# Optimization experiments

Hardware: AMD Instinct MI355X
Metric: run time of the kernel (lower is better)

The kernel has to match this reference:

```python
import jax, jax.numpy as jnp
import numpy as np

P = 16          # patch size (patch_height == patch_width)
DIM = 768       # feature dim
K = 9           # number of anchor boxes (arange(0, 9) in source)
# anchor_boxes = [(h_ratio, w_ratio) for h in (2,4,8) for w in (2,4,8)]
BOX_H = jnp.array([2., 2., 2., 4., 4., 4., 8., 8., 8.], dtype=jnp.float32)
BOX_W = jnp.array([2., 4., 8., 2., 4., 8., 2., 4., 8.], dtype=jnp.float32)


def setup_inputs() -> dict:
    key = jax.random.key(0)
    k0, k1, k2, k3 = jax.random.split(key, 4)
    b, c, h, w = 32, 3, 512, 512
    img = jax.random.normal(k0, (b, c, h, w), dtype=jnp.float32)
    # patch-embed stand-in for feature_extraction_ViT: (c*P*P) -> DIM
    w_patch = jax.random.normal(k1, (c * P * P, DIM), dtype=jnp.float32) * 0.02
    w_reg = jax.random.normal(k2, (DIM, 4 * K), dtype=jnp.float32) * 0.02
    b_reg = jnp.zeros((4 * K,), dtype=jnp.float32)
    w_obj = jax.random.normal(k3, (DIM, K), dtype=jnp.float32) * 0.02
    b_obj = jnp.zeros((K,), dtype=jnp.float32)
    return {"img": img, "w_patch": w_patch, "w_reg": w_reg, "b_reg": b_reg,
            "w_obj": w_obj, "b_obj": b_obj}


def reference(img, w_patch, w_reg, b_reg, w_obj, b_obj):
    b, c, h, w = img.shape
    fh, fw = h // P, w // P
    # --- feature_extraction_ViT (patch embedding) -> feature map [b, fh, fw, DIM]
    patches = img.reshape(b, c, fh, P, fw, P).transpose(0, 2, 4, 1, 3, 5)
    patches = patches.reshape(b, fh, fw, c * P * P)
    feat = patches @ w_patch                                  # [b, fh, fw, DIM]
    # --- RPN: regs [b, fh, fw, K, 4], objectness [b, fh, fw, K, 1]
    regs = (feat @ w_reg + b_reg).reshape(b, fh, fw, K, 4)    # separate_anchor_boxes, s=4
    is_object = jax.nn.sigmoid(feat @ w_obj + b_obj)[..., None]
    # --- anchor-box coordinate decoding (memory-bound broadcast pipeline)
    wgrid = jnp.arange(0, w, P, dtype=jnp.float32)            # step = patch_width
    hgrid = jnp.arange(0, h, P, dtype=jnp.float32)            # step = patch_height
    width_coords = wgrid[None, None, :, None, None] + regs[..., 0:1]
    height_coords = hgrid[None, :, None, None, None] + regs[..., 1:2]
    width_abs = width_coords + BOX_W[None, None, None, :, None] * regs[..., 2:3]
    height_abs = height_coords + BOX_H[None, None, None, :, None] * regs[..., 3:4]
    batch_idx = jnp.broadcast_to(
        jnp.arange(b, dtype=jnp.float32)[:, None, None, None, None], (b, fh, fw, K, 1))
    k_idx = jnp.broadcast_to(
        jnp.arange(K, dtype=jnp.float32)[None, None, None, :, None], (b, fh, fw, K, 1))
    merged = jnp.concatenate(
        [width_coords, height_coords, width_abs, height_abs, batch_idx, is_object, k_idx],
        axis=-1)                                              # [b, fh, fw, K, 7]
    tensor_reshaped = merged.reshape(-1, 7)                   # (b h w k) x
    return tensor_reshaped
```

## Files before the change

kernel.cpp:

```cpp
#include <hip/hip_runtime.h>

typedef __attribute__((ext_vector_type(8))) short bf16x8;
typedef __attribute__((ext_vector_type(4))) float f32x4;

__device__ __forceinline__ unsigned short f2bf(float f) {
    unsigned int u = __float_as_uint(f);
    u = (u + 0x7FFFu + ((u >> 16) & 1u)) >> 16;
    return (unsigned short)u;
}

__global__ __launch_bounds__(256) void btrans(
        const float* __restrict__ wreg, const float* __restrict__ wobj,
        float* __restrict__ Bt) {
    const int idx = blockIdx.x * 256 + threadIdx.x;
    const int n = idx / 768, d = idx - n * 768;
    float v = 0.f;
    if (n < 36)      v = wreg[(size_t)d * 36 + n];
    else if (n < 45) v = wobj[(size_t)d * 9 + (n - 36)];
    Bt[idx] = v;
}

__global__ __launch_bounds__(256) void wcomb_partial2(
        const float* __restrict__ wp, const float* __restrict__ Bt,
        float* __restrict__ part) {
    __shared__ float Al[16][132];
    __shared__ float Bl[48][132];
    const int t  = threadIdx.x;
    const int kb = blockIdx.x * 16;
    const int dc = blockIdx.y;
    const int d0 = dc * 128;

    #pragma unroll
    for (int i = 0; i < 2; ++i) {
        int e = i * 256 + t;
        int row = e >> 5, v = e & 31;
        *(f32x4*)&Al[row][v * 4] =
            *(const f32x4*)&wp[(size_t)(kb + row) * 768 + d0 + v * 4];
    }
    #pragma unroll
    for (int i = 0; i < 6; ++i) {
        int e = i * 256 + t;
        int row = e >> 5, v = e & 31;
        *(f32x4*)&Bl[row][v * 4] =
            *(const f32x4*)&Bt[(size_t)row * 768 + d0 + v * 4];
    }
    __syncthreads();

    const int k  = t >> 4;
    const int n0 = (t & 15) * 3;
    float acc[3] = {0.f, 0.f, 0.f};
    #pragma unroll 8
    for (int ds = 0; ds < 32; ++ds) {
        f32x4 a = *(const f32x4*)&Al[k][ds * 4];
        #pragma unroll
        for (int j = 0; j < 3; ++j) {
            f32x4 b = *(const f32x4*)&Bl[n0 + j][ds * 4];
            acc[j] += a.x * b.x + a.y * b.y + a.z * b.z + a.w * b.w;
        }
    }
    #pragma unroll
    for (int j = 0; j < 3; ++j)
        part[((size_t)dc * 768 + kb + k) * 48 + n0 + j] = acc[j];
}

__global__ __launch_bounds__(256) void wcomb_reduce2(
        const float* __restrict__ part, unsigned short* __restrict__ wct) {
    const int idx = blockIdx.x * 256 + threadIdx.x;
    const int n = idx / 768, k = idx - n * 768;
    float s = 0.f;
    if (n < 45) {
        #pragma unroll
        for (int dc = 0; dc < 6; ++dc) s += part[((size_t)dc * 768 + k) * 48 + n];
    }
    wct[idx] = f2bf(s);
}

__global__ __launch_bounds__(256) void detector_main(
        const float* __restrict__ img, const unsigned short* __restrict__ wct,
        const float* __restrict__ breg, const float* __restrict__ bobj,
        float* __restrict__ out) {
    __shared__ float Co[4][16][49];

    const int t    = threadIdx.x;
    const int lane = t & 63;
    const int wid  = t >> 6;
    const int cl   = lane & 15;
    const int q    = lane >> 4;
    const int kh   = wid & 1;
    const int tg   = blockIdx.x * 2 + (wid >> 1);
    const int fj0  = (tg & 1) * 16;
    const int fi   = (tg >> 1) & 31;
    const int b    = tg >> 6;

    const float* ap = img + (size_t)b * 786432 + (size_t)kh * 266240
        + (size_t)(fi * 16 + (q >> 1)) * 512 + (fj0 + cl) * 16 + (q & 1) * 8;
    const unsigned short* bp = wct + cl * 768 + q * 8 + kh * 384;

    f32x4 acc0 = {0.f,0.f,0.f,0.f}, acc1 = acc0, acc2 = acc0;

    f32x4 ca0 = *(const f32x4*)ap;
    f32x4 ca1 = *(const f32x4*)(ap + 4);
    bf16x8 cb0 = *(const bf16x8*)(bp);
    bf16x8 cb1 = *(const bf16x8*)(bp + 12288);
    bf16x8 cb2 = *(const bf16x8*)(bp + 24576);

    #pragma unroll 4
    for (int i = 0; i < 12; ++i) {
        const int kk = kh * 12 + i;
        const int astep = ((kk & 7) == 7) ? 254976 : 1024;
        const float* nap = (i == 11) ? ap : ap + astep;
        const unsigned short* nbp = (i == 11) ? bp : bp + 32;
        f32x4 na0 = *(const f32x4*)nap;
        f32x4 na1 = *(const f32x4*)(nap + 4);
        bf16x8 nb0 = *(const bf16x8*)(nbp);
        bf16x8 nb1 = *(const bf16x8*)(nbp + 12288);
        bf16x8 nb2 = *(const bf16x8*)(nbp + 24576);

        bf16x8 af;
        af[0] = (short)f2bf(ca0.x); af[1] = (short)f2bf(ca0.y);
        af[2] = (short)f2bf(ca0.z); af[3] = (short)f2bf(ca0.w);
        af[4] = (short)f2bf(ca1.x); af[5] = (short)f2bf(ca1.y);
        af[6] = (short)f2bf(ca1.z); af[7] = (short)f2bf(ca1.w);
        acc0 = __builtin_amdgcn_mfma_f32_16x16x32_bf16(af, cb0, acc0, 0, 0, 0);
        acc1 = __builtin_amdgcn_mfma_f32_16x16x32_bf16(af, cb1, acc1, 0, 0, 0);
        acc2 = __builtin_amdgcn_mfma_f32_16x16x32_bf16(af, cb2, acc2, 0, 0, 0);

        ap = nap; bp = nbp;
        ca0 = na0; ca1 = na1; cb0 = nb0; cb1 = nb1; cb2 = nb2;
    }

    #pragma unroll
    for (int r = 0; r < 4; ++r) {
        Co[wid][q * 4 + r][ 0 + cl] = acc0[r];
        Co[wid][q * 4 + r][16 + cl] = acc1[r];
        Co[wid][q * 4 + r][32 + cl] = acc2[r];
    }
    __syncthreads();

    for (int rr = t; rr < 288; rr += 256) {
        int tp   = rr / 144;
        int rw   = rr - tp * 144;
        int cell = rw / 9, k = rw - cell * 9;
        int tgd  = blockIdx.x * 2 + tp;
        int dfj  = (tgd & 1) * 16 + cell;
        int dfi  = (tgd >> 1) & 31;
        int db   = tgd >> 6;
        float v0 = Co[2*tp][cell][4*k+0] + Co[2*tp+1][cell][4*k+0] + breg[4*k+0];
        float v1 = Co[2*tp][cell][4*k+1] + Co[2*tp+1][cell][4*k+1] + breg[4*k+1];
        float v2 = Co[2*tp][cell][4*k+2] + Co[2*tp+1][cell][4*k+2] + breg[4*k+2];
        float v3 = Co[2*tp][cell][4*k+3] + Co[2*tp+1][cell][4*k+3] + breg[4*k+3];
        float lg = Co[2*tp][cell][36+k]  + Co[2*tp+1][cell][36+k]  + bobj[k];
        float obj = 1.f / (1.f + __expf(-lg));
        float wc = (float)(dfj * 16) + v0;
        float hc = (float)(dfi * 16) + v1;
        float wa = wc + (float)(2 << (k % 3)) * v2;
        float ha = hc + (float)(2 << (k / 3)) * v3;
        float* o = out + (size_t)(((db * 32 + dfi) * 32 + dfj) * 9 + k) * 7;
        o[0] = wc; o[1] = hc; o[2] = wa; o[3] = ha;
        o[4] = (float)db; o[5] = obj; o[6] = (float)k;
    }
}

extern "C" void kernel_launch(void* const* d_in, const int* in_sizes, int n_in,
                              void* d_out, int out_size, void* d_ws, size_t ws_size,
                              hipStream_t stream) {
    const float* img  = (const float*)d_in[0];
    const float* wp   = (const float*)d_in[1];
    const float* wreg = (const float*)d_in[2];
    const float* breg = (const float*)d_in[3];
    const float* wobj = (const float*)d_in[4];
    const float* bobj = (const float*)d_in[5];
    float* out = (float*)d_out;

    unsigned short* wct = (unsigned short*)d_ws;
    float* Bt   = (float*)((char*)d_ws + 73728);
    float* part = (float*)((char*)d_ws + 73728 + 147456);

    btrans<<<144, 256, 0, stream>>>(wreg, wobj, Bt);
    wcomb_partial2<<<dim3(48, 6), 256, 0, stream>>>(wp, Bt, part);
    wcomb_reduce2<<<144, 256, 0, stream>>>(part, wct);
    detector_main<<<1024, 256, 0, stream>>>(img, wct, breg, bobj, out);
}
```

Before: 174.8 us.

## Split K across four waves per tile, deepen prefetch, pack bf16 conversion

Each block now handles a single 16-cell tile, with its four waves each taking a quarter of the K dimension (6 steps) rather than two waves each taking half. The grid doubles to 2048 blocks, which raises parallelism and memory-level parallelism for the image-streaming GEMM. A/B loads are prefetched two steps ahead for A and one step ahead for B, and fp32-to-bf16 conversion goes through the packed __float22bfloat162_rn intrinsic. The cost is a four-way LDS reduction in the epilogue and fewer output rows written per block, so more blocks do less epilogue work each.

```diff
diff --git a/kernel.cpp b/kernel.cpp
--- a/kernel.cpp
+++ b/kernel.cpp
@@ -1,4 +1,5 @@
 #include <hip/hip_runtime.h>
+#include <hip/hip_bf16.h>
 
 typedef __attribute__((ext_vector_type(8))) short bf16x8;
 typedef __attribute__((ext_vector_type(4))) float f32x4;
@@ -7,6 +8,13 @@
     unsigned int u = __float_as_uint(f);
     u = (u + 0x7FFFu + ((u >> 16) & 1u)) >> 16;
     return (unsigned short)u;
+}
+
+__device__ __forceinline__ unsigned int pkbf(float x, float y) {
+    __hip_bfloat162 h = __float22bfloat162_rn(float2{x, y});
+    unsigned int u;
+    __builtin_memcpy(&u, &h, 4);
+    return u;
 }
 
 __global__ __launch_bounds__(256) void btrans(
@@ -86,48 +94,55 @@
     const int wid  = t >> 6;
     const int cl   = lane & 15;
     const int q    = lane >> 4;
-    const int kh   = wid & 1;
-    const int tg   = blockIdx.x * 2 + (wid >> 1);
+    const int tg   = blockIdx.x;
     const int fj0  = (tg & 1) * 16;
     const int fi   = (tg >> 1) & 31;
     const int b    = tg >> 6;
+    const int k0   = wid * 6;
 
-    const float* ap = img + (size_t)b * 786432 + (size_t)kh * 266240
+    const float* abase = img + (size_t)b * 786432
         + (size_t)(fi * 16 + (q >> 1)) * 512 + (fj0 + cl) * 16 + (q & 1) * 8;
-    const unsigned short* bp = wct + cl * 768 + q * 8 + kh * 384;
+    const unsigned short* bbase = wct + cl * 768 + q * 8;
+
+    #define AOFF(kk) ((size_t)((kk) >> 3) * 262144 + (size_t)((kk) & 7) * 1024)
 
     f32x4 acc0 = {0.f,0.f,0.f,0.f}, acc1 = acc0, acc2 = acc0;
 
-    f32x4 ca0 = *(const f32x4*)ap;
-    f32x4 ca1 = *(const f32x4*)(ap + 4);
-    bf16x8 cb0 = *(const bf16x8*)(bp);
-    bf16x8 cb1 = *(const bf16x8*)(bp + 12288);
-    bf16x8 cb2 = *(const bf16x8*)(bp + 24576);
+    f32x4 a0lo = *(const f32x4*)(abase + AOFF(k0));
+    f32x4 a0hi = *(const f32x4*)(abase + AOFF(k0) + 4);
+    f32x4 a1lo = *(const f32x4*)(abase + AOFF(k0 + 1));
+    f32x4 a1hi = *(const f32x4*)(abase + AOFF(k0 + 1) + 4);
+    bf16x8 b0x = *(const bf16x8*)(bbase + (size_t)k0 * 32);
+    bf16x8 b0y = *(const bf16x8*)(bbase + (size_t)k0 * 32 + 12288);
+    bf16x8 b0z = *(const bf16x8*)(bbase + (size_t)k0 * 32 + 24576);
 
-    #pragma unroll 4
-    for (int i = 0; i < 12; ++i) {
-        const int kk = kh * 12 + i;
-        const int astep = ((kk & 7) == 7) ? 254976 : 1024;
-        const float* nap = (i == 11) ? ap : ap + astep;
-        const unsigned short* nbp = (i == 11) ? bp : bp + 32;
-        f32x4 na0 = *(const f32x4*)nap;
-        f32x4 na1 = *(const f32x4*)(nap + 4);
-        bf16x8 nb0 = *(const bf16x8*)(nbp);
-        bf16x8 nb1 = *(const bf16x8*)(nbp + 12288);
-        bf16x8 nb2 = *(const bf16x8*)(nbp + 24576);
+    #pragma unroll
+    for (int i = 0; i < 6; ++i) {
+        f32x4 a2lo, a2hi;
+        if (i < 4) {
+            a2lo = *(const f32x4*)(abase + AOFF(k0 + i + 2));
+            a2hi = *(const f32x4*)(abase + AOFF(k0 + i + 2) + 4);
+        } else { a2lo = a1lo; a2hi = a1hi; }
+        bf16x8 b1x, b1y, b1z;
+        if (i < 5) {
+            b1x = *(const bf16x8*)(bbase + (size_t)(k0 + i + 1) * 32);
+            b1y = *(const bf16x8*)(bbase + (size_t)(k0 + i + 1) * 32 + 12288);
+            b1z = *(const bf16x8*)(bbase + (size_t)(k0 + i + 1) * 32 + 24576);
+        } else { b1x = b0x; b1y = b0y; b1z = b0z; }
 
-        bf16x8 af;
-        af[0] = (short)f2bf(ca0.x); af[1] = (short)f2bf(ca0.y);
-        af[2] = (short)f2bf(ca0.z); af[3] = (short)f2bf(ca0.w);
-        af[4] = (short)f2bf(ca1.x); af[5] = (short)f2bf(ca1.y);
-        af[6] = (short)f2bf(ca1.z); af[7] = (short)f2bf(ca1.w);
-        acc0 = __builtin_amdgcn_mfma_f32_16x16x32_bf16(af, cb0, acc0, 0, 0, 0);
-        acc1 = __builtin_amdgcn_mfma_f32_16x16x32_bf16(af, cb1, acc1, 0, 0, 0);
-        acc2 = __builtin_amdgcn_mfma_f32_16x16x32_bf16(af, cb2, acc2, 0, 0, 0);
+        union { bf16x8 v; unsigned int u[4]; } af;
+        af.u[0] = pkbf(a0lo.x, a0lo.y);
+        af.u[1] = pkbf(a0lo.z, a0lo.w);
+        af.u[2] = pkbf(a0hi.x, a0hi.y);
+        af.u[3] = pkbf(a0hi.z, a0hi.w);
+        acc0 = __builtin_amdgcn_mfma_f32_16x16x32_bf16(af.v, b0x, acc0, 0, 0, 0);
+        acc1 = __builtin_amdgcn_mfma_f32_16x16x32_bf16(af.v, b0y, acc1, 0, 0, 0);
+        acc2 = __builtin_amdgcn_mfma_f32_16x16x32_bf16(af.v, b0z, acc2, 0, 0, 0);
 
-        ap = nap; bp = nbp;
-        ca0 = na0; ca1 = na1; cb0 = nb0; cb1 = nb1; cb2 = nb2;
+        a0lo = a1lo; a0hi = a1hi; a1lo = a2lo; a1hi = a2hi;
+        b0x = b1x; b0y = b1y; b0z = b1z;
     }
+    #undef AOFF
 
     #pragma unroll
     for (int r = 0; r < 4; ++r) {
@@ -137,27 +152,27 @@
     }
     __syncthreads();
 
-    for (int rr = t; rr < 288; rr += 256) {
-        int tp   = rr / 144;
-        int rw   = rr - tp * 144;
-        int cell = rw / 9, k = rw - cell * 9;
-        int tgd  = blockIdx.x * 2 + tp;
-        int dfj  = (tgd & 1) * 16 + cell;
-        int dfi  = (tgd >> 1) & 31;
-        int db   = tgd >> 6;
-        float v0 = Co[2*tp][cell][4*k+0] + Co[2*tp+1][cell][4*k+0] + breg[4*k+0];
-        float v1 = Co[2*tp][cell][4*k+1] + Co[2*tp+1][cell][4*k+1] + breg[4*k+1];
-        float v2 = Co[2*tp][cell][4*k+2] + Co[2*tp+1][cell][4*k+2] + breg[4*k+2];
-        float v3 = Co[2*tp][cell][4*k+3] + Co[2*tp+1][cell][4*k+3] + breg[4*k+3];
-        float lg = Co[2*tp][cell][36+k]  + Co[2*tp+1][cell][36+k]  + bobj[k];
+    for (int rr = t; rr < 144; rr += 256) {
+        int cell = rr / 9, k = rr - cell * 9;
+        int dfj  = fj0 + cell;
+        float v0 = Co[0][cell][4*k+0] + Co[1][cell][4*k+0]
+                 + Co[2][cell][4*k+0] + Co[3][cell][4*k+0] + breg[4*k+0];
+        float v1 = Co[0][cell][4*k+1] + Co[1][cell][4*k+1]
+                 + Co[2][cell][4*k+1] + Co[3][cell][4*k+1] + breg[4*k+1];
+        float v2 = Co[0][cell][4*k+2] + Co[1][cell][4*k+2]
+                 + Co[2][cell][4*k+2] + Co[3][cell][4*k+2] + breg[4*k+2];
+        float v3 = Co[0][cell][4*k+3] + Co[1][cell][4*k+3]
+                 + Co[2][cell][4*k+3] + Co[3][cell][4*k+3] + breg[4*k+3];
+        float lg = Co[0][cell][36+k]  + Co[1][cell][36+k]
+                 + Co[2][cell][36+k]  + Co[3][cell][36+k]  + bobj[k];
         float obj = 1.f / (1.f + __expf(-lg));
         float wc = (float)(dfj * 16) + v0;
-        float hc = (float)(dfi * 16) + v1;
+        float hc = (float)(fi * 16) + v1;
         float wa = wc + (float)(2 << (k % 3)) * v2;
         float ha = hc + (float)(2 << (k / 3)) * v3;
-        float* o = out + (size_t)(((db * 32 + dfi) * 32 + dfj) * 9 + k) * 7;
+        float* o = out + (size_t)(((b * 32 + fi) * 32 + dfj) * 9 + k) * 7;
         o[0] = wc; o[1] = hc; o[2] = wa; o[3] = ha;
-        o[4] = (float)db; o[5] = obj; o[6] = (float)k;
+        o[4] = (float)b; o[5] = obj; o[6] = (float)k;
     }
 }
 
@@ -179,5 +194,5 @@
     btrans<<<144, 256, 0, stream>>>(wreg, wobj, Bt);
     wcomb_partial2<<<dim3(48, 6), 256, 0, stream>>>(wp, Bt, part);
     wcomb_reduce2<<<144, 256, 0, stream>>>(part, wct);
-    detector_main<<<1024, 256, 0, stream>>>(img, wct, breg, bobj, out);
+    detector_main<<<2048, 256, 0, stream>>>(img, wct, breg, bobj, out);
 }
```

After: 174.7 us, median of 2. Within noise of the previous version (-0.0%).
